# Performance work log

Measured on AMD Instinct MI355X. Metric: run time of the kernel, lower is better.

## Reference

```python
import jax, jax.numpy as jnp
import numpy as np

N_NODES = 100000
N_EDGES = 800000
F_IN = 128
C_HID = 32
N_CLS = 16
K_HOPS = 3
CST = 1e-05


def setup_inputs() -> dict:
    key = jax.random.key(0)
    ks = jax.random.split(key, 12)
    node_feat = jax.random.normal(ks[0], (N_NODES, F_IN), dtype=jnp.float32)
    edge_index = jax.random.randint(ks[1], (2, N_EDGES), 0, N_NODES, dtype=jnp.int64)
    def lin(k, fan_in, fan_out):
        bound = 1.0 / np.sqrt(fan_in)
        kw, kb = jax.random.split(k)
        W = jax.random.uniform(kw, (fan_in, fan_out), minval=-bound, maxval=bound, dtype=jnp.float32)
        b = jax.random.uniform(kb, (fan_out,), minval=-bound, maxval=bound, dtype=jnp.float32)
        return W, b
    W_in, b_in = lin(ks[2], F_IN, C_HID)
    Wq, bq = lin(ks[3], C_HID, C_HID)
    Wk, bk = lin(ks[4], C_HID, C_HID)
    Wv, bv = lin(ks[5], C_HID, N_CLS)
    hopwise = jnp.ones((K_HOPS + 1,), dtype=jnp.float32)
    return {"node_feat": node_feat, "edge_index": edge_index,
            "W_in": W_in, "b_in": b_in, "Wq": Wq, "bq": bq,
            "Wk": Wk, "bk": bk, "Wv": Wv, "bv": bv, "hopwise": hopwise}


def reference(node_feat, edge_index, W_in, b_in, Wq, bq, Wk, bk, Wv, bv, hopwise):
    n = node_feat.shape[0]
    row, col = edge_index[0], edge_index[1]  # messages flow row -> col (PyG source_to_target)
    x = jax.nn.relu(node_feat @ W_in + b_in)            # [n, c]
    Q = 1.0 + jax.nn.elu(x @ Wq + bq)                    # [n, c]
    K = 1.0 + jax.nn.elu(x @ Wk + bk)                    # [n, c]
    V = x @ Wv + bv                                      # [n, d]
    M = jnp.einsum('ni,nj->nij', K, V)                   # [n, c, d]
    hidden = V * hopwise[0]
    for hop in range(K_HOPS):
        # scatter-sum aggregation over edges (aggr='add')
        M = jax.ops.segment_sum(M[row], col, num_segments=n)  # [n, c, d]
        K = jax.ops.segment_sum(K[row], col, num_segments=n)  # [n, c]
        H = jnp.einsum('ni,nij->nj', Q, M)               # [n, d]
        C = jnp.einsum('ni,ni->n', Q, K)[:, None] + CST  # [n, 1]
        hidden = hidden + hopwise[hop + 1] * (H / C)
    return hidden
```

## Files before the change

### kernel.cpp

```cpp
#include <hip/hip_runtime.h>
#include <math.h>

#define NN 100000
#define NE 800000
#define F_IN 128
#define CH 32
#define NC 16
#define CSTF 1e-5f
#define CAP 48

typedef float v2f __attribute__((ext_vector_type(2)));
typedef float v4f __attribute__((ext_vector_type(4)));
typedef short v8s __attribute__((ext_vector_type(8)));

__device__ __forceinline__ float bf_lo(unsigned int u) {
    unsigned int t = u << 16;
    return __builtin_bit_cast(float, t);
}
__device__ __forceinline__ float bf_hi(unsigned int u) {
    unsigned int t = u & 0xffff0000u;
    return __builtin_bit_cast(float, t);
}
__device__ __forceinline__ float bf_val(unsigned short v) {
    unsigned int t = ((unsigned int)v) << 16;
    return __builtin_bit_cast(float, t);
}
__device__ __forceinline__ v2f bf_pair(unsigned int u) {
    v2f r; r.x = bf_lo(u); r.y = bf_hi(u); return r;
}
__device__ __forceinline__ unsigned int bf_round(float a) {
    unsigned int ua = __builtin_bit_cast(unsigned int, a);
    return (ua + 0x7fffu + ((ua >> 16) & 1u)) >> 16;
}
__device__ __forceinline__ short bfq(float a) {
    unsigned int ua = __builtin_bit_cast(unsigned int, a);
    return (short)((ua + 0x8000u) >> 16);
}
__device__ __forceinline__ unsigned int bf_pack2(float a, float b) {
    return bf_round(a) | (bf_round(b) << 16);
}

__device__ __forceinline__ float cl448(float a) {
    return fminf(fmaxf(a, -448.f), 448.f);
}

__device__ __forceinline__ float elu1(float x) {
    return 1.f + ((x > 0.f) ? x : (expf(x) - 1.f));
}

__global__ void zero_kernel(int* __restrict__ p, int n) {
    int i = blockIdx.x * 256 + threadIdx.x;
    if (i < n) p[i] = 0;
}

__global__ void detect_kernel(const int* __restrict__ ei, int* __restrict__ mode) {
    __shared__ int any_nz;
    if (threadIdx.x == 0) any_nz = 0;
    __syncthreads();
    int nz = 0;
    for (int i = threadIdx.x; i < 4096; i += 256) nz |= (ei[2 * i + 1] != 0);
    if (nz) atomicOr(&any_nz, 1);
    __syncthreads();
    if (threadIdx.x == 0) *mode = any_nz ? 0 : 1;
}

__device__ __forceinline__ int get_row(const int* ei, int e, int m) {
    return m ? ei[2 * e] : ei[e];
}
__device__ __forceinline__ int get_col(const int* ei, int e, int m) {
    return m ? ei[2 * NE + 2 * e] : ei[NE + e];
}

__global__ void fillb_kernel(const int* __restrict__ ei, int* __restrict__ deg,
                             int* __restrict__ srcs, const int* __restrict__ mode) {
    int e = blockIdx.x * 256 + threadIdx.x;
    int m = *mode;
    if (e < NE) {
        int c = get_col(ei, e, m);
        int p = atomicAdd(&deg[c], 1);
        if (p < CAP) srcs[(size_t)c * CAP + p] = get_row(ei, e, m);
    }
}

__global__ __launch_bounds__(256) void phase1_kernel(
    const float* __restrict__ feat, const float* __restrict__ Win,
    const float* __restrict__ bin, const float* __restrict__ Wq,
    const float* __restrict__ bq, const float* __restrict__ Wk,
    const float* __restrict__ bk, const float* __restrict__ Wv,
    const float* __restrict__ bv, const float* __restrict__ hopwise,
    float* __restrict__ Qg, unsigned short* __restrict__ Kb,
    unsigned short* __restrict__ Vb, float* __restrict__ out)
{
    __shared__ float xs_all[4][16 * 36];

    int tid  = threadIdx.x;
    int wid  = tid >> 6;
    int lane = tid & 63;
    int q    = lane >> 4;
    int col  = lane & 15;
    int node0 = (blockIdx.x * 4 + wid) * 16;

    v8s wb[4][2];
#pragma unroll
    for (int kk = 0; kk < 4; ++kk)
#pragma unroll
        for (int t = 0; t < 2; ++t)
#pragma unroll
            for (int j = 0; j < 8; ++j)
                wb[kk][t][j] = (short)bf_round(Win[(kk * 32 + q * 8 + j) * CH + t * 16 + col]);

    v8s wq[2], wk[2], wv;
#pragma unroll
    for (int t = 0; t < 2; ++t)
#pragma unroll
        for (int j = 0; j < 8; ++j) {
            wq[t][j] = (short)bf_round(Wq[(q * 8 + j) * CH + t * 16 + col]);
            wk[t][j] = (short)bf_round(Wk[(q * 8 + j) * CH + t * 16 + col]);
        }
#pragma unroll
    for (int j = 0; j < 8; ++j)
        wv[j] = (short)bf_round(Wv[(q * 8 + j) * NC + col]);

    float bin0 = bin[col], bin1 = bin[col + 16];
    float bq0 = bq[col], bq1 = bq[col + 16];
    float bk0 = bk[col], bk1 = bk[col + 16];
    float bv0 = bv[col];
    float hw0 = hopwise[0];

    int nodeA = node0 + col;
    int nclamp = nodeA < NN ? nodeA : NN - 1;
    const float* fr = feat + (size_t)nclamp * F_IN + q * 8;

    v4f acc0 = {0.f, 0.f, 0.f, 0.f}, acc1 = {0.f, 0.f, 0.f, 0.f};
#pragma unroll
    for (int kk = 0; kk < 4; ++kk) {
        float4 a = *(const float4*)(fr + kk * 32);
        float4 b = *(const float4*)(fr + kk * 32 + 4);
        v8s af;
        af[0] = bfq(a.x); af[1] = bfq(a.y); af[2] = bfq(a.z); af[3] = bfq(a.w);
        af[4] = bfq(b.x); af[5] = bfq(b.y); af[6] = bfq(b.z); af[7] = bfq(b.w);
        acc0 = __builtin_amdgcn_mfma_f32_16x16x32_bf16(af, wb[kk][0], acc0, 0, 0, 0);
        acc1 = __builtin_amdgcn_mfma_f32_16x16x32_bf16(af, wb[kk][1], acc1, 0, 0, 0);
    }

    float* xs = xs_all[wid];
#pragma unroll
    for (int r = 0; r < 4; ++r) {
        xs[(q * 4 + r) * 36 + col]      = fmaxf(acc0[r] + bin0, 0.f);
        xs[(q * 4 + r) * 36 + col + 16] = fmaxf(acc1[r] + bin1, 0.f);
    }

    float4 xa = *(const float4*)&xs[col * 36 + q * 8];
    float4 xb = *(const float4*)&xs[col * 36 + q * 8 + 4];
    v8s xf;
    xf[0] = bfq(xa.x); xf[1] = bfq(xa.y); xf[2] = bfq(xa.z); xf[3] = bfq(xa.w);
    xf[4] = bfq(xb.x); xf[5] = bfq(xb.y); xf[6] = bfq(xb.z); xf[7] = bfq(xb.w);

    v4f aq0 = {0.f,0.f,0.f,0.f}, aq1 = {0.f,0.f,0.f,0.f};
    v4f ak0 = {0.f,0.f,0.f,0.f}, ak1 = {0.f,0.f,0.f,0.f};
    v4f av  = {0.f,0.f,0.f,0.f};
    aq0 = __builtin_amdgcn_mfma_f32_16x16x32_bf16(xf, wq[0], aq0, 0, 0, 0);
    aq1 = __builtin_amdgcn_mfma_f32_16x16x32_bf16(xf, wq[1], aq1, 0, 0, 0);
    ak0 = __builtin_amdgcn_mfma_f32_16x16x32_bf16(xf, wk[0], ak0, 0, 0, 0);
    ak1 = __builtin_amdgcn_mfma_f32_16x16x32_bf16(xf, wk[1], ak1, 0, 0, 0);
    av  = __builtin_amdgcn_mfma_f32_16x16x32_bf16(xf, wv,    av,  0, 0, 0);

#pragma unroll
    for (int r = 0; r < 4; ++r) {
        int nd = node0 + 4 * q + r;
        if (nd < NN) {
            float q0 = elu1(aq0[r] + bq0);
            float q1 = elu1(aq1[r] + bq1);
            float k0 = elu1(ak0[r] + bk0);
            float k1 = elu1(ak1[r] + bk1);
            float vv = av[r] + bv0;
            Qg[(size_t)nd * CH + col]      = q0;
            Qg[(size_t)nd * CH + col + 16] = q1;
            Kb[(size_t)nd * CH + col]      = (unsigned short)bf_round(k0);
            Kb[(size_t)nd * CH + col + 16] = (unsigned short)bf_round(k1);
            Vb[(size_t)nd * NC + col]      = (unsigned short)bf_round(vv);
            out[(size_t)nd * NC + col]     = hw0 * vv;
        }
    }
}

__global__ __launch_bounds__(256) void hopA_kernel(
    const float* __restrict__ Qg, const unsigned short* __restrict__ Kb,
    const unsigned short* __restrict__ Vb,
    unsigned char* __restrict__ Mout, unsigned short* __restrict__ Kout,
    const int* __restrict__ deg, const int* __restrict__ srcs,
    const float* __restrict__ hopw, float* __restrict__ out)
{
    int tid  = threadIdx.x;
    int wid  = tid >> 6;
    int lane = tid & 63;
    int node = __builtin_amdgcn_readfirstlane(blockIdx.x * 4 + wid);
    int jB   = lane >> 2;
    int s4   = lane & 3;
    int cseg = s4 * 8;

    v2f acc2[4];
#pragma unroll
    for (int t = 0; t < 4; ++t) { acc2[t].x = 0.f; acc2[t].y = 0.f; }
    v2f kagg2[4];
#pragma unroll
    for (int t = 0; t < 4; ++t) { kagg2[t].x = 0.f; kagg2[t].y = 0.f; }

    int d = deg[node];
    if (d > CAP) d = CAP;
    const int* sl = srcs + (size_t)node * CAP;
    int i = 0;

    for (; i + 3 < d; i += 4) {
        int s0 = sl[i], s1 = sl[i+1], s2 = sl[i+2], s3 = sl[i+3];
        uint4 kr0 = *(const uint4*)(Kb + (size_t)s0 * CH + cseg);
        uint4 kr1 = *(const uint4*)(Kb + (size_t)s1 * CH + cseg);
        uint4 kr2 = *(const uint4*)(Kb + (size_t)s2 * CH + cseg);
        uint4 kr3 = *(const uint4*)(Kb + (size_t)s3 * CH + cseg);
        float vj0 = bf_val(Vb[(size_t)s0 * NC + jB]);
        float vj1 = bf_val(Vb[(size_t)s1 * NC + jB]);
        float vj2 = bf_val(Vb[(size_t)s2 * NC + jB]);
        float vj3 = bf_val(Vb[(size_t)s3 * NC + jB]);
        v2f k;
        k = bf_pair(kr0.x); kagg2[0] += k; acc2[0] += k * vj0;
        k = bf_pair(kr0.y); kagg2[1] += k; acc2[1] += k * vj0;
        k = bf_pair(kr0.z); kagg2[2] += k; acc2[2] += k * vj0;
        k = bf_pair(kr0.w); kagg2[3] += k; acc2[3] += k * vj0;
        k = bf_pair(kr1.x); kagg2[0] += k; acc2[0] += k * vj1;
        k = bf_pair(kr1.y); kagg2[1] += k; acc2[1] += k * vj1;
        k = bf_pair(kr1.z); kagg2[2] += k; acc2[2] += k * vj1;
        k = bf_pair(kr1.w); kagg2[3] += k; acc2[3] += k * vj1;
        k = bf_pair(kr2.x); kagg2[0] += k; acc2[0] += k * vj2;
        k = bf_pair(kr2.y); kagg2[1] += k; acc2[1] += k * vj2;
        k = bf_pair(kr2.z); kagg2[2] += k; acc2[2] += k * vj2;
        k = bf_pair(kr2.w); kagg2[3] += k; acc2[3] += k * vj2;
        k = bf_pair(kr3.x); kagg2[0] += k; acc2[0] += k * vj3;
        k = bf_pair(kr3.y); kagg2[1] += k; acc2[1] += k * vj3;
        k = bf_pair(kr3.z); kagg2[2] += k; acc2[2] += k * vj3;
        k = bf_pair(kr3.w); kagg2[3] += k; acc2[3] += k * vj3;
    }
    for (; i < d; ++i) {
        int s0 = sl[i];
        uint4 kr0 = *(const uint4*)(Kb + (size_t)s0 * CH + cseg);
        float vj0 = bf_val(Vb[(size_t)s0 * NC + jB]);
        v2f k;
        k = bf_pair(kr0.x); kagg2[0] += k; acc2[0] += k * vj0;
        k = bf_pair(kr0.y); kagg2[1] += k; acc2[1] += k * vj0;
        k = bf_pair(kr0.z); kagg2[2] += k; acc2[2] += k * vj0;
        k = bf_pair(kr0.w); kagg2[3] += k; acc2[3] += k * vj0;
    }

    const float4* qp = (const float4*)(Qg + (size_t)node * CH + cseg);
    float4 qa = qp[0], qb = qp[1];
    v2f q2[4];
    q2[0].x = qa.x; q2[0].y = qa.y; q2[1].x = qa.z; q2[1].y = qa.w;
    q2[2].x = qb.x; q2[2].y = qb.y; q2[3].x = qb.z; q2[3].y = qb.w;

    v2f t = q2[0] * kagg2[0] + q2[1] * kagg2[1]
          + q2[2] * kagg2[2] + q2[3] * kagg2[3];
    float cpv = t.x + t.y;
    cpv += __shfl_xor(cpv, 1);
    cpv += __shfl_xor(cpv, 2);
    float sc = hopw[1] / (cpv + CSTF);

    if (lane < 4) {
        uint4 kw;
        kw.x = bf_pack2(kagg2[0].x, kagg2[0].y);
        kw.y = bf_pack2(kagg2[1].x, kagg2[1].y);
        kw.z = bf_pack2(kagg2[2].x, kagg2[2].y);
        kw.w = bf_pack2(kagg2[3].x, kagg2[3].y);
        *(uint4*)(Kout + (size_t)node * CH + cseg) = kw;
    }
    int p0 = 0, p1 = 0;
    p0 = __builtin_amdgcn_cvt_pk_fp8_f32(cl448(acc2[0].x), cl448(acc2[0].y), p0, false);
    p0 = __builtin_amdgcn_cvt_pk_fp8_f32(cl448(acc2[1].x), cl448(acc2[1].y), p0, true);
    p1 = __builtin_amdgcn_cvt_pk_fp8_f32(cl448(acc2[2].x), cl448(acc2[2].y), p1, false);
    p1 = __builtin_amdgcn_cvt_pk_fp8_f32(cl448(acc2[3].x), cl448(acc2[3].y), p1, true);
    uint2 u; u.x = (unsigned int)p0; u.y = (unsigned int)p1;
    *(uint2*)(Mout + (size_t)node * 512 + lane * 8) = u;

    v2f h2 = q2[0] * acc2[0] + q2[1] * acc2[1]
           + q2[2] * acc2[2] + q2[3] * acc2[3];
    float hp = h2.x + h2.y;
    hp += __shfl_xor(hp, 1);
    hp += __shfl_xor(hp, 2);

    if (s4 == 0)
        out[(size_t)node * NC + jB] += sc * hp;
}

#define PAIRB(SA, SB) { \
    int s_ = half ? (SB) : (SA); \
    uint4 u_ = *(const uint4*)(Min + (size_t)s_ * 512 + hl * 16); \
    kagg += bf_val(Kb[(size_t)s_ * CH + hl]); \
    acc2[0] += (v2f)__builtin_amdgcn_cvt_pk_f32_fp8(u_.x, false); \
    acc2[1] += (v2f)__builtin_amdgcn_cvt_pk_f32_fp8(u_.x, true);  \
    acc2[2] += (v2f)__builtin_amdgcn_cvt_pk_f32_fp8(u_.y, false); \
    acc2[3] += (v2f)__builtin_amdgcn_cvt_pk_f32_fp8(u_.y, true);  \
    acc2[4] += (v2f)__builtin_amdgcn_cvt_pk_f32_fp8(u_.z, false); \
    acc2[5] += (v2f)__builtin_amdgcn_cvt_pk_f32_fp8(u_.z, true);  \
    acc2[6] += (v2f)__builtin_amdgcn_cvt_pk_f32_fp8(u_.w, false); \
    acc2[7] += (v2f)__builtin_amdgcn_cvt_pk_f32_fp8(u_.w, true);  \
}

template<bool WRITE>
__global__ __launch_bounds__(256) void hopM_kernel(
    const float* __restrict__ Qg, const unsigned short* __restrict__ Kb,
    const unsigned char* __restrict__ Min,
    unsigned char* __restrict__ Mout, unsigned short* __restrict__ Kout,
    const int* __restrict__ deg, const int* __restrict__ srcs,
    const float* __restrict__ hopw, int hop, float* __restrict__ out)
{
    int tid  = threadIdx.x;
    int wid  = tid >> 6;
    int lane = tid & 63;
    int node = __builtin_amdgcn_readfirstlane(blockIdx.x * 4 + wid);
    int half = lane >> 5;
    int hl   = lane & 31;

    v2f acc2[8];
#pragma unroll
    for (int t = 0; t < 8; ++t) { acc2[t].x = 0.f; acc2[t].y = 0.f; }
    float kagg = 0.f;

    int d = deg[node];
    if (d > CAP) d = CAP;
    const int* sl = srcs + (size_t)node * CAP;
    int i = 0;

    for (; i + 7 < d; i += 8) {
        int s0 = sl[i],   s1 = sl[i+1], s2 = sl[i+2], s3 = sl[i+3];
        int s4_ = sl[i+4], s5 = sl[i+5], s6 = sl[i+6], s7 = sl[i+7];
        PAIRB(s0, s1);
        PAIRB(s2, s3);
        PAIRB(s4_, s5);
        PAIRB(s6, s7);
    }
    for (; i + 1 < d; i += 2) {
        int sa = sl[i], sb = sl[i+1];
        PAIRB(sa, sb);
    }
    if (i < d) {
        int s_ = sl[i];
        uint4 u_ = *(const uint4*)(Min + (size_t)s_ * 512 + hl * 16);
        float kv = bf_val(Kb[(size_t)s_ * CH + hl]);
        if (half) { u_.x = 0u; u_.y = 0u; u_.z = 0u; u_.w = 0u; kv = 0.f; }
        kagg += kv;
        acc2[0] += (v2f)__builtin_amdgcn_cvt_pk_f32_fp8(u_.x, false);
        acc2[1] += (v2f)__builtin_amdgcn_cvt_pk_f32_fp8(u_.x, true);
        acc2[2] += (v2f)__builtin_amdgcn_cvt_pk_f32_fp8(u_.y, false);
        acc2[3] += (v2f)__builtin_amdgcn_cvt_pk_f32_fp8(u_.y, true);
        acc2[4] += (v2f)__builtin_amdgcn_cvt_pk_f32_fp8(u_.z, false);
        acc2[5] += (v2f)__builtin_amdgcn_cvt_pk_f32_fp8(u_.z, true);
        acc2[6] += (v2f)__builtin_amdgcn_cvt_pk_f32_fp8(u_.w, false);
        acc2[7] += (v2f)__builtin_amdgcn_cvt_pk_f32_fp8(u_.w, true);
    }

#pragma unroll
    for (int t = 0; t < 8; ++t) {
        acc2[t].x += __shfl_xor(acc2[t].x, 32);
        acc2[t].y += __shfl_xor(acc2[t].y, 32);
    }
    kagg += __shfl_xor(kagg, 32);

    float qcl = Qg[(size_t)node * CH + hl];
    float cpv = qcl * kagg;
#pragma unroll
    for (int st = 1; st <= 16; st <<= 1) cpv += __shfl_xor(cpv, st);
    float sc = hopw[hop] / (cpv + CSTF);

    if (WRITE) {
        if (half == 0) {
            Kout[(size_t)node * CH + hl] = (unsigned short)bf_round(kagg);
            int p0 = 0, p1 = 0, p2 = 0, p3 = 0;
            p0 = __builtin_amdgcn_cvt_pk_fp8_f32(cl448(acc2[0].x), cl448(acc2[0].y), p0, false);
            p0 = __builtin_amdgcn_cvt_pk_fp8_f32(cl448(acc2[1].x), cl448(acc2[1].y), p0, true);
            p1 = __builtin_amdgcn_cvt_pk_fp8_f32(cl448(acc2[2].x), cl448(acc2[2].y), p1, false);
            p1 = __builtin_amdgcn_cvt_pk_fp8_f32(cl448(acc2[3].x), cl448(acc2[3].y), p1, true);
            p2 = __builtin_amdgcn_cvt_pk_fp8_f32(cl448(acc2[4].x), cl448(acc2[4].y), p2, false);
            p2 = __builtin_amdgcn_cvt_pk_fp8_f32(cl448(acc2[5].x), cl448(acc2[5].y), p2, true);
            p3 = __builtin_amdgcn_cvt_pk_fp8_f32(cl448(acc2[6].x), cl448(acc2[6].y), p3, false);
            p3 = __builtin_amdgcn_cvt_pk_fp8_f32(cl448(acc2[7].x), cl448(acc2[7].y), p3, true);
            uint4 w;
            w.x = (unsigned int)p0; w.y = (unsigned int)p1;
            w.z = (unsigned int)p2; w.w = (unsigned int)p3;
            *(uint4*)(Mout + (size_t)node * 512 + hl * 16) = w;
        }
    }

    const float4* qp = (const float4*)(Qg + (size_t)node * CH + (hl & 1) * 16);
    float4 qa = qp[0], qb = qp[1], qcq = qp[2], qd = qp[3];
    float hp = qa.x * acc2[0].x + qa.y * acc2[0].y
             + qa.z * acc2[1].x + qa.w * acc2[1].y
             + qb.x * acc2[2].x + qb.y * acc2[2].y
             + qb.z * acc2[3].x + qb.w * acc2[3].y
             + qcq.x * acc2[4].x + qcq.y * acc2[4].y
             + qcq.z * acc2[5].x + qcq.w * acc2[5].y
             + qd.x * acc2[6].x + qd.y * acc2[6].y
             + qd.z * acc2[7].x + qd.w * acc2[7].y;
    hp += __shfl_xor(hp, 1);

    if (half == 0 && (hl & 1) == 0)
        out[(size_t)node * NC + (hl >> 1)] += sc * hp;
}

extern "C" void kernel_launch(void* const* d_in, const int* in_sizes, int n_in,
                              void* d_out, int out_size, void* d_ws, size_t ws_size,
                              hipStream_t stream) {
    const float* feat = (const float*)d_in[0];
    const int*   ei   = (const int*)d_in[1];
    const float* Win  = (const float*)d_in[2];
    const float* bin  = (const float*)d_in[3];
    const float* Wq   = (const float*)d_in[4];
    const float* bq   = (const float*)d_in[5];
    const float* Wk   = (const float*)d_in[6];
    const float* bk   = (const float*)d_in[7];
    const float* Wv   = (const float*)d_in[8];
    const float* bv   = (const float*)d_in[9];
    const float* hopw = (const float*)d_in[10];
    float* out = (float*)d_out;

    char* ws = (char*)d_ws;
    size_t off = 0;
    auto alloc = [&](size_t bytes) -> void* {
        void* p = ws + off;
        off += (bytes + 255) & ~(size_t)255;
        return p;
    };
    float*          Qg  = (float*)alloc((size_t)NN * CH * 4);
    unsigned short* K0b = (unsigned short*)alloc((size_t)NN * CH * 2);
    unsigned short* K1b = (unsigned short*)alloc((size_t)NN * CH * 2);
    unsigned short* K2b = (unsigned short*)alloc((size_t)NN * CH * 2);
    unsigned short* Vb  = (unsigned short*)alloc((size_t)NN * NC * 2);
    int*   deg  = (int*)alloc((size_t)NN * 4);
    int*   mode = (int*)alloc(4);
    int*   srcs = (int*)alloc((size_t)NN * CAP * 4);
    unsigned char* MA = (unsigned char*)alloc((size_t)NN * 512);
    unsigned char* MB = (unsigned char*)alloc((size_t)NN * 512);

    zero_kernel<<<(NN + 255) / 256, 256, 0, stream>>>(deg, NN);
    detect_kernel<<<1, 256, 0, stream>>>(ei, mode);
    fillb_kernel<<<(NE + 255) / 256, 256, 0, stream>>>(ei, deg, srcs, mode);

    phase1_kernel<<<1563, 256, 0, stream>>>(feat, Win, bin, Wq, bq, Wk, bk, Wv, bv,
                                            hopw, Qg, K0b, Vb, out);

    hopA_kernel<<<25000, 256, 0, stream>>>(Qg, K0b, Vb, MA, K1b, deg, srcs, hopw, out);
    hopM_kernel<true ><<<25000, 256, 0, stream>>>(Qg, K1b, MA, MB, K2b, deg, srcs, hopw, 2, out);
    hopM_kernel<false><<<25000, 256, 0, stream>>>(Qg, K2b, MB, nullptr, nullptr, deg, srcs, hopw, 3, out);
}
```

Baseline: 408.1 us.

## Gather full M rows per lane with 8-byte loads and batched edge prefetch

The per-node hop kernel now has each of the 64 lanes gather 8 bytes of a neighbor's FP8 M row, instead of two half-waves each loading 16 bytes of different neighbors. This removes the cross-half shuffle reduction, and every lane does useful work in the final store. Edge loads are issued in batches of 8 and 4 before any accumulation, to raise memory-level parallelism. The 1-3 edge tail is handled with clamped indices and zero weights. Each lane now issues more, smaller loads, and the Q dot product is reduced over 4 lanes instead of 2.

```diff
diff --git a/kernel.cpp b/kernel.cpp
--- a/kernel.cpp
+++ b/kernel.cpp
@@ -289,20 +289,6 @@
         out[(size_t)node * NC + jB] += sc * hp;
 }
 
-#define PAIRB(SA, SB) { \
-    int s_ = half ? (SB) : (SA); \
-    uint4 u_ = *(const uint4*)(Min + (size_t)s_ * 512 + hl * 16); \
-    kagg += bf_val(Kb[(size_t)s_ * CH + hl]); \
-    acc2[0] += (v2f)__builtin_amdgcn_cvt_pk_f32_fp8(u_.x, false); \
-    acc2[1] += (v2f)__builtin_amdgcn_cvt_pk_f32_fp8(u_.x, true);  \
-    acc2[2] += (v2f)__builtin_amdgcn_cvt_pk_f32_fp8(u_.y, false); \
-    acc2[3] += (v2f)__builtin_amdgcn_cvt_pk_f32_fp8(u_.y, true);  \
-    acc2[4] += (v2f)__builtin_amdgcn_cvt_pk_f32_fp8(u_.z, false); \
-    acc2[5] += (v2f)__builtin_amdgcn_cvt_pk_f32_fp8(u_.z, true);  \
-    acc2[6] += (v2f)__builtin_amdgcn_cvt_pk_f32_fp8(u_.w, false); \
-    acc2[7] += (v2f)__builtin_amdgcn_cvt_pk_f32_fp8(u_.w, true);  \
-}
-
 template<bool WRITE>
 __global__ __launch_bounds__(256) void hopM_kernel(
     const float* __restrict__ Qg, const unsigned short* __restrict__ Kb,
@@ -315,12 +301,18 @@
     int wid  = tid >> 6;
     int lane = tid & 63;
     int node = __builtin_amdgcn_readfirstlane(blockIdx.x * 4 + wid);
-    int half = lane >> 5;
-    int hl   = lane & 31;
-
-    v2f acc2[8];
-#pragma unroll
-    for (int t = 0; t < 8; ++t) { acc2[t].x = 0.f; acc2[t].y = 0.f; }
+    int jB   = lane >> 2;
+    int s4   = lane & 3;
+    int cseg = s4 * 8;
+    int c32  = lane & 31;
+
+    float qcl = Qg[(size_t)node * CH + c32];
+    const float4* qp = (const float4*)(Qg + (size_t)node * CH + cseg);
+    float4 qa = qp[0], qb = qp[1];
+
+    v2f acc2[4];
+#pragma unroll
+    for (int t = 0; t < 4; ++t) { acc2[t].x = 0.f; acc2[t].y = 0.f; }
     float kagg = 0.f;
 
     int d = deg[node];
@@ -328,80 +320,91 @@
     const int* sl = srcs + (size_t)node * CAP;
     int i = 0;
 
-    for (; i + 7 < d; i += 8) {
-        int s0 = sl[i],   s1 = sl[i+1], s2 = sl[i+2], s3 = sl[i+3];
-        int s4_ = sl[i+4], s5 = sl[i+5], s6 = sl[i+6], s7 = sl[i+7];
-        PAIRB(s0, s1);
-        PAIRB(s2, s3);
-        PAIRB(s4_, s5);
-        PAIRB(s6, s7);
-    }
-    for (; i + 1 < d; i += 2) {
-        int sa = sl[i], sb = sl[i+1];
-        PAIRB(sa, sb);
+    for (; i + 8 <= d; i += 8) {
+        uint2 u[8]; float kv[8];
+#pragma unroll
+        for (int j = 0; j < 8; ++j) {
+            int s_ = sl[i + j];
+            u[j]  = *(const uint2*)(Min + (size_t)s_ * 512 + lane * 8);
+            kv[j] = bf_val(Kb[(size_t)s_ * CH + c32]);
+        }
+#pragma unroll
+        for (int j = 0; j < 8; ++j) {
+            kagg += kv[j];
+            acc2[0] += (v2f)__builtin_amdgcn_cvt_pk_f32_fp8(u[j].x, false);
+            acc2[1] += (v2f)__builtin_amdgcn_cvt_pk_f32_fp8(u[j].x, true);
+            acc2[2] += (v2f)__builtin_amdgcn_cvt_pk_f32_fp8(u[j].y, false);
+            acc2[3] += (v2f)__builtin_amdgcn_cvt_pk_f32_fp8(u[j].y, true);
+        }
+    }
+    if (i + 4 <= d) {
+        uint2 u[4]; float kv[4];
+#pragma unroll
+        for (int j = 0; j < 4; ++j) {
+            int s_ = sl[i + j];
+            u[j]  = *(const uint2*)(Min + (size_t)s_ * 512 + lane * 8);
+            kv[j] = bf_val(Kb[(size_t)s_ * CH + c32]);
+        }
+#pragma unroll
+        for (int j = 0; j < 4; ++j) {
+            kagg += kv[j];
+            acc2[0] += (v2f)__builtin_amdgcn_cvt_pk_f32_fp8(u[j].x, false);
+            acc2[1] += (v2f)__builtin_amdgcn_cvt_pk_f32_fp8(u[j].x, true);
+            acc2[2] += (v2f)__builtin_amdgcn_cvt_pk_f32_fp8(u[j].y, false);
+            acc2[3] += (v2f)__builtin_amdgcn_cvt_pk_f32_fp8(u[j].y, true);
+        }
+        i += 4;
     }
     if (i < d) {
-        int s_ = sl[i];
-        uint4 u_ = *(const uint4*)(Min + (size_t)s_ * 512 + hl * 16);
-        float kv = bf_val(Kb[(size_t)s_ * CH + hl]);
-        if (half) { u_.x = 0u; u_.y = 0u; u_.z = 0u; u_.w = 0u; kv = 0.f; }
-        kagg += kv;
-        acc2[0] += (v2f)__builtin_amdgcn_cvt_pk_f32_fp8(u_.x, false);
-        acc2[1] += (v2f)__builtin_amdgcn_cvt_pk_f32_fp8(u_.x, true);
-        acc2[2] += (v2f)__builtin_amdgcn_cvt_pk_f32_fp8(u_.y, false);
-        acc2[3] += (v2f)__builtin_amdgcn_cvt_pk_f32_fp8(u_.y, true);
-        acc2[4] += (v2f)__builtin_amdgcn_cvt_pk_f32_fp8(u_.z, false);
-        acc2[5] += (v2f)__builtin_amdgcn_cvt_pk_f32_fp8(u_.z, true);
-        acc2[6] += (v2f)__builtin_amdgcn_cvt_pk_f32_fp8(u_.w, false);
-        acc2[7] += (v2f)__builtin_amdgcn_cvt_pk_f32_fp8(u_.w, true);
-    }
-
-#pragma unroll
-    for (int t = 0; t < 8; ++t) {
-        acc2[t].x += __shfl_xor(acc2[t].x, 32);
-        acc2[t].y += __shfl_xor(acc2[t].y, 32);
-    }
-    kagg += __shfl_xor(kagg, 32);
-
-    float qcl = Qg[(size_t)node * CH + hl];
+        uint2 u[3]; float kv[3]; float w[3];
+#pragma unroll
+        for (int j = 0; j < 3; ++j) {
+            int ii  = i + j;
+            int iic = ii < d ? ii : d - 1;
+            int s_  = sl[iic];
+            u[j]  = *(const uint2*)(Min + (size_t)s_ * 512 + lane * 8);
+            kv[j] = bf_val(Kb[(size_t)s_ * CH + c32]);
+            w[j]  = (ii < d) ? 1.f : 0.f;
+        }
+#pragma unroll
+        for (int j = 0; j < 3; ++j) {
+            kagg = fmaf(kv[j], w[j], kagg);
+            v2f c;
+            c = (v2f)__builtin_amdgcn_cvt_pk_f32_fp8(u[j].x, false); acc2[0] += c * w[j];
+            c = (v2f)__builtin_amdgcn_cvt_pk_f32_fp8(u[j].x, true);  acc2[1] += c * w[j];
+            c = (v2f)__builtin_amdgcn_cvt_pk_f32_fp8(u[j].y, false); acc2[2] += c * w[j];
+            c = (v2f)__builtin_amdgcn_cvt_pk_f32_fp8(u[j].y, true);  acc2[3] += c * w[j];
+        }
+    }
+
     float cpv = qcl * kagg;
 #pragma unroll
     for (int st = 1; st <= 16; st <<= 1) cpv += __shfl_xor(cpv, st);
     float sc = hopw[hop] / (cpv + CSTF);
 
     if (WRITE) {
-        if (half == 0) {
-            Kout[(size_t)node * CH + hl] = (unsigned short)bf_round(kagg);
-            int p0 = 0, p1 = 0, p2 = 0, p3 = 0;
-            p0 = __builtin_amdgcn_cvt_pk_fp8_f32(cl448(acc2[0].x), cl448(acc2[0].y), p0, false);
-            p0 = __builtin_amdgcn_cvt_pk_fp8_f32(cl448(acc2[1].x), cl448(acc2[1].y), p0, true);
-            p1 = __builtin_amdgcn_cvt_pk_fp8_f32(cl448(acc2[2].x), cl448(acc2[2].y), p1, false);
-            p1 = __builtin_amdgcn_cvt_pk_fp8_f32(cl448(acc2[3].x), cl448(acc2[3].y), p1, true);
-            p2 = __builtin_amdgcn_cvt_pk_fp8_f32(cl448(acc2[4].x), cl448(acc2[4].y), p2, false);
-            p2 = __builtin_amdgcn_cvt_pk_fp8_f32(cl448(acc2[5].x), cl448(acc2[5].y), p2, true);
-            p3 = __builtin_amdgcn_cvt_pk_fp8_f32(cl448(acc2[6].x), cl448(acc2[6].y), p3, false);
-            p3 = __builtin_amdgcn_cvt_pk_fp8_f32(cl448(acc2[7].x), cl448(acc2[7].y), p3, true);
-            uint4 w;
-            w.x = (unsigned int)p0; w.y = (unsigned int)p1;
-            w.z = (unsigned int)p2; w.w = (unsigned int)p3;
-            *(uint4*)(Mout + (size_t)node * 512 + hl * 16) = w;
-        }
-    }
-
-    const float4* qp = (const float4*)(Qg + (size_t)node * CH + (hl & 1) * 16);
-    float4 qa = qp[0], qb = qp[1], qcq = qp[2], qd = qp[3];
-    float hp = qa.x * acc2[0].x + qa.y * acc2[0].y
-             + qa.z * acc2[1].x + qa.w * acc2[1].y
-             + qb.x * acc2[2].x + qb.y * acc2[2].y
-             + qb.z * acc2[3].x + qb.w * acc2[3].y
-             + qcq.x * acc2[4].x + qcq.y * acc2[4].y
-             + qcq.z * acc2[5].x + qcq.w * acc2[5].y
-             + qd.x * acc2[6].x + qd.y * acc2[6].y
-             + qd.z * acc2[7].x + qd.w * acc2[7].y;
+        if (lane < 32)
+            Kout[(size_t)node * CH + c32] = (unsigned short)bf_round(kagg);
+        int p0 = 0, p1 = 0;
+        p0 = __builtin_amdgcn_cvt_pk_fp8_f32(cl448(acc2[0].x), cl448(acc2[0].y), p0, false);
+        p0 = __builtin_amdgcn_cvt_pk_fp8_f32(cl448(acc2[1].x), cl448(acc2[1].y), p0, true);
+        p1 = __builtin_amdgcn_cvt_pk_fp8_f32(cl448(acc2[2].x), cl448(acc2[2].y), p1, false);
+        p1 = __builtin_amdgcn_cvt_pk_fp8_f32(cl448(acc2[3].x), cl448(acc2[3].y), p1, true);
+        uint2 u; u.x = (unsigned int)p0; u.y = (unsigned int)p1;
+        *(uint2*)(Mout + (size_t)node * 512 + lane * 8) = u;
+    }
+
+    v2f q2[4];
+    q2[0].x = qa.x; q2[0].y = qa.y; q2[1].x = qa.z; q2[1].y = qa.w;
+    q2[2].x = qb.x; q2[2].y = qb.y; q2[3].x = qb.z; q2[3].y = qb.w;
+    v2f h2 = q2[0] * acc2[0] + q2[1] * acc2[1]
+           + q2[2] * acc2[2] + q2[3] * acc2[3];
+    float hp = h2.x + h2.y;
     hp += __shfl_xor(hp, 1);
-
-    if (half == 0 && (hl & 1) == 0)
-        out[(size_t)node * NC + (hl >> 1)] += sc * hp;
+    hp += __shfl_xor(hp, 2);
+
+    if (s4 == 0)
+        out[(size_t)node * NC + jB] += sc * hp;
 }
 
 extern "C" void kernel_launch(void* const* d_in, const int* in_sizes, int n_in,
```

New measurement: 391.7 us. 4.0% less time.
